# Performance work log

Measured on AMD Instinct MI355X. Metric: run time of the kernel, lower is better.

## Reference

```python
import jax, jax.numpy as jnp
import numpy as np

TWO_PI = 6.283185307179586


def setup_inputs() -> dict:
    key = jax.random.key(0)
    k1, k2, k3, k4, k5, k6 = jax.random.split(key, 6)
    B, T, D = 2, 8192, 1024
    x = jax.random.normal(k1, (B, T, D), dtype=jnp.float32)
    # nn.Linear weights are [out, in]; init with small scale like torch default
    s = 1.0 / np.sqrt(D)
    Wk = jax.random.uniform(k2, (D, D), jnp.float32, -s, s)
    Wv = jax.random.uniform(k3, (D, D), jnp.float32, -s, s)
    Wo = jax.random.uniform(k4, (D, D), jnp.float32, -s, s)
    # random phasor frequencies in [0, 2*pi)
    freqs = jax.random.uniform(k5, (D,), jnp.float32, 0.0, TWO_PI)
    return {"x": x, "Wk": Wk, "Wv": Wv, "Wo": Wo, "freqs": freqs}


def reference(x, Wk, Wv, Wo, freqs):
    B, T, C = x.shape
    # k projection is computed in the original forward but never used downstream
    k_real = x @ Wk.T  # [B,T,D] (dead value, kept for fidelity)
    v_real = x @ Wv.T  # [B,T,D]
    v = v_real.astype(jnp.complex64)
    # rotors: per-position unit phasors exp(i * t * freqs), shape [T, D]
    t = jnp.arange(T, dtype=jnp.float32)
    rotors = jnp.exp(1j * (t[:, None] * freqs[None, :])).astype(jnp.complex64)
    # bind each value with its rotor and accumulate causally (O(N) memory trace)
    memory_trace = jnp.cumsum(v * rotors[None, :, :], axis=1)  # [B,T,D] complex64
    # retrieve by unbinding with the conjugate rotor; take the real component
    retrieved = jnp.real(memory_trace * jnp.conj(rotors)[None, :, :])  # [B,T,D]
    return retrieved @ Wo.T
```

## Files before the change

### kernel.cpp

```cpp
#include <hip/hip_runtime.h>
#include <hip/hip_bf16.h>


#define B_  2
#define T_  8192
#define D_  1024
#define BT_ 16384
#define CS_ 64
#define NCHUNK_ 128

typedef __attribute__((ext_vector_type(4))) float f32x4;
typedef __attribute__((ext_vector_type(8))) short bf16x8;

static __device__ inline unsigned short f2bf(float f) {
    union { float f; unsigned int u; } a;
    a.f = f;
    unsigned int u = a.u;
    return (unsigned short)((u + 0x7FFFu + ((u >> 16) & 1u)) >> 16);
}
static __device__ inline float bf2f(unsigned short h) {
    union { unsigned int u; float f; } a;
    a.u = ((unsigned int)h) << 16;
    return a.f;
}

__global__ __launch_bounds__(256) void cast_all(const float* __restrict__ x,
                                                const float* __restrict__ Wv,
                                                const float* __restrict__ Wo,
                                                unsigned short* __restrict__ xb,
                                                unsigned short* __restrict__ wvb,
                                                unsigned short* __restrict__ wob) {
    const int nx = BT_ * D_ / 4;
    const int nw = D_ * D_ / 4;
    int i = blockIdx.x * 256 + threadIdx.x;
    const float4* src;
    unsigned short* dst;
    int j;
    if (i < nx)            { src = (const float4*)x;  dst = xb;  j = i; }
    else if (i < nx + nw)  { src = (const float4*)Wv; dst = wvb; j = i - nx; }
    else                   { src = (const float4*)Wo; dst = wob; j = i - nx - nw; }
    float4 v = src[j];
    ushort4 o;
    o.x = f2bf(v.x); o.y = f2bf(v.y); o.z = f2bf(v.z); o.w = f2bf(v.w);
    ((ushort4*)dst)[j] = o;
}

template <bool BF16OUT, bool FUSE_SUMS>
__global__ __launch_bounds__(256) void gemm_bt(const short* __restrict__ A,
                                               const short* __restrict__ Bm,
                                               void* __restrict__ Cout,
                                               const float* __restrict__ freqs,
                                               float* __restrict__ csum,
                                               int M, int N, int K) {
    __shared__ short lds[16384];
    const int lane = threadIdx.x & 63;
    const int wave = threadIdx.x >> 6;
    const int wr = wave >> 1, wc = wave & 1;

    const int nb = N >> 7;
    const int id = blockIdx.x;
    const int xcd = id & 7;
    const int slot = id >> 3;
    const int bn = (slot % nb) * 128;
    const int bm = (xcd * ((M >> 7) >> 3) + slot / nb) * 128;

    const int sr = lane >> 3;
    const int cb = lane & 7;
    const short* ga[4];
    const short* gb[4];
#pragma unroll
    for (int cc = 0; cc < 4; ++cc) {
        const int chunk = wave * 4 + cc;
        const int row = chunk * 8 + sr;
        const int col = (cb ^ (row & 7)) * 8;
        ga[cc] = A + (size_t)(bm + row) * K + col;
        gb[cc] = Bm + (size_t)(bn + row) * K + col;
    }

    const int c4r = lane >> 4;
    int aoff[4][2], boff[4][2];
#pragma unroll
    for (int i = 0; i < 4; ++i) {
        const int m = wr * 64 + (lane & 15) + i * 16;
        const int n = wc * 64 + (lane & 15) + i * 16;
#pragma unroll
        for (int ks = 0; ks < 2; ++ks) {
            aoff[i][ks] = m * 64 + (((ks * 4 + c4r) ^ (m & 7)) * 8);
            boff[i][ks] = 8192 + n * 64 + (((ks * 4 + c4r) ^ (n & 7)) * 8);
        }
    }

    f32x4 acc[4][4] = {};

    for (int k0 = 0; k0 < K; k0 += 64) {
#pragma unroll
        for (int cc = 0; cc < 4; ++cc) {
            const int chunk = wave * 4 + cc;
            __builtin_amdgcn_global_load_lds(
                (const __attribute__((address_space(1))) void*)(ga[cc] + k0),
                (__attribute__((address_space(3))) void*)&lds[chunk * 512], 16, 0, 0);
            __builtin_amdgcn_global_load_lds(
                (const __attribute__((address_space(1))) void*)(gb[cc] + k0),
                (__attribute__((address_space(3))) void*)&lds[8192 + chunk * 512], 16, 0, 0);
        }
        __syncthreads();
#pragma unroll
        for (int ks = 0; ks < 2; ++ks) {
            bf16x8 a[4], b[4];
#pragma unroll
            for (int i = 0; i < 4; ++i) a[i] = *(const bf16x8*)&lds[aoff[i][ks]];
#pragma unroll
            for (int j = 0; j < 4; ++j) b[j] = *(const bf16x8*)&lds[boff[j][ks]];
#pragma unroll
            for (int i = 0; i < 4; ++i)
#pragma unroll
                for (int j = 0; j < 4; ++j)
                    acc[i][j] = __builtin_amdgcn_mfma_f32_16x16x32_bf16(a[i], b[j], acc[i][j], 0, 0, 0);
        }
        __syncthreads();
    }

    const int row0 = c4r * 4;
#pragma unroll
    for (int i = 0; i < 4; ++i) {
#pragma unroll
        for (int j = 0; j < 4; ++j) {
            const int col = bn + wc * 64 + j * 16 + (lane & 15);
#pragma unroll
            for (int r = 0; r < 4; ++r) {
                const size_t row = bm + wr * 64 + i * 16 + row0 + r;
                if constexpr (BF16OUT)
                    ((unsigned short*)Cout)[row * N + col] = f2bf(acc[i][j][r]);
                else
                    ((float*)Cout)[row * N + col] = acc[i][j][r];
            }
        }
    }

    if constexpr (FUSE_SUMS) {
        const int b = bm >> 13;
        const int trow = bm & 8191;
        const int chunk = (trow >> 6) + wr;
        const int t0 = trow + wr * 64 + c4r * 4;
#pragma unroll
        for (int j = 0; j < 4; ++j) {
            const int d = bn + wc * 64 + j * 16 + (lane & 15);
            const float f = freqs[d];
            float ss, cc2;
            sincosf((float)t0 * f, &ss, &cc2);
            float s1, c1;
            sincosf(f, &s1, &c1);
            float c2 = c1 * c1 - s1 * s1, s2 = 2.f * c1 * s1;
            float c4 = c2 * c2 - s2 * s2, s4 = 2.f * c2 * s2;
            float c8 = c4 * c4 - s4 * s4, s8 = 2.f * c4 * s4;
            float c12 = c8 * c4 - s8 * s4, s12 = s8 * c4 + c8 * s4;
            float c13 = c12 * c1 - s12 * s1, s13 = s12 * c1 + c12 * s1;
            float ar = 0.f, ai = 0.f;
            float cr = cc2, sr2 = ss;
#pragma unroll
            for (int i = 0; i < 4; ++i) {
#pragma unroll
                for (int r = 0; r < 4; ++r) {
                    const float w = acc[i][j][r];
                    ar = fmaf(w, cr, ar); ai = fmaf(w, sr2, ai);
                    const float ec = (r < 3) ? c1 : c13;
                    const float es = (r < 3) ? s1 : s13;
                    const float nc = cr * ec - sr2 * es;
                    const float ns = sr2 * ec + cr * es;
                    cr = nc; sr2 = ns;
                }
            }
            ar += __shfl_xor(ar, 16); ai += __shfl_xor(ai, 16);
            ar += __shfl_xor(ar, 32); ai += __shfl_xor(ai, 32);
            if (c4r == 0)
                *(float2*)(csum + (((size_t)b * NCHUNK_ + chunk) * D_ + d) * 2) =
                    make_float2(ar, ai);
        }
    }
}

__global__ __launch_bounds__(256) void scan_pass2(float* __restrict__ csum) {
    const int g = blockIdx.x * 256 + threadIdx.x;
    const int b = g / D_;
    const int d = g % D_;
    float2* cs = (float2*)csum;
    const size_t base = (size_t)b * NCHUNK_ * D_ + d;
    float pr = 0.f, pi = 0.f;
    for (int cc = 0; cc < NCHUNK_; cc += 32) {
        float2 buf[32];
#pragma unroll
        for (int k = 0; k < 32; ++k) buf[k] = cs[base + (size_t)(cc + k) * D_];
#pragma unroll
        for (int k = 0; k < 32; ++k) {
            float r = buf[k].x, im = buf[k].y;
            buf[k] = make_float2(pr, pi);
            pr += r; pi += im;
        }
#pragma unroll
        for (int k = 0; k < 32; ++k) cs[base + (size_t)(cc + k) * D_] = buf[k];
    }
}

__global__ __launch_bounds__(256) void scan_pass3(const unsigned short* __restrict__ v,
                                                  const float* __restrict__ freqs,
                                                  const float* __restrict__ csum,
                                                  unsigned short* __restrict__ ret) {
    const int chunk = blockIdx.x;
    const int d0 = blockIdx.y * 512 + threadIdx.x * 2;
    const int b = blockIdx.z;

    float fr[2], s[2], c[2], sf[2], cf[2], ar[2], ai[2];
    {
        float2 f2 = *(const float2*)(freqs + d0);
        fr[0] = f2.x; fr[1] = f2.y;
    }
    const float t0f = (float)(chunk * CS_);
#pragma unroll
    for (int k = 0; k < 2; ++k) {
        sincosf(t0f * fr[k], &s[k], &c[k]);
        sincosf(fr[k], &sf[k], &cf[k]);
    }
    {
        const float4 o = *(const float4*)(csum + (((size_t)b * NCHUNK_ + chunk) * D_ + d0) * 2);
        ar[0] = o.x; ai[0] = o.y; ar[1] = o.z; ai[1] = o.w;
    }
    const unsigned int* vp = (const unsigned int*)(v + ((size_t)b * T_ + chunk * CS_) * D_ + d0);
    unsigned int* rp = (unsigned int*)(ret + ((size_t)b * T_ + chunk * CS_) * D_ + d0);
    for (int tb = 0; tb < CS_; tb += 8) {
        unsigned int w[8];
#pragma unroll
        for (int u = 0; u < 8; ++u) w[u] = vp[(size_t)(tb + u) * (D_ / 2)];
#pragma unroll
        for (int u = 0; u < 8; ++u) {
            float wv[2], o[2];
            wv[0] = bf2f((unsigned short)w[u]);
            wv[1] = bf2f((unsigned short)(w[u] >> 16));
#pragma unroll
            for (int k = 0; k < 2; ++k) {
                ar[k] = fmaf(wv[k], c[k], ar[k]);
                ai[k] = fmaf(wv[k], s[k], ai[k]);
                o[k] = ar[k] * c[k] + ai[k] * s[k];
                float nc = c[k] * cf[k] - s[k] * sf[k];
                float ns = s[k] * cf[k] + c[k] * sf[k];
                c[k] = nc; s[k] = ns;
            }
            rp[(size_t)(tb + u) * (D_ / 2)] =
                (unsigned int)f2bf(o[0]) | ((unsigned int)f2bf(o[1]) << 16);
        }
    }
}

extern "C" void kernel_launch(void* const* d_in, const int* in_sizes, int n_in,
                              void* d_out, int out_size, void* d_ws, size_t ws_size,
                              hipStream_t stream) {
    const float* x     = (const float*)d_in[0];
    const float* Wv    = (const float*)d_in[2];
    const float* Wo    = (const float*)d_in[3];
    const float* freqs = (const float*)d_in[4];
    float* out = (float*)d_out;

    char* ws = (char*)d_ws;
    unsigned short* x_bf  = (unsigned short*)ws;
    unsigned short* Wv_bf = (unsigned short*)(ws + 33554432);
    unsigned short* Wo_bf = (unsigned short*)(ws + 35651584);
    unsigned short* ret   = (unsigned short*)(ws + 37748736);
    float*          csum  = (float*)(ws + 71303168);
    unsigned short* v_bf = (unsigned short*)d_out;

    cast_all<<<(BT_ * D_ / 4 + 2 * D_ * D_ / 4) / 256, 256, 0, stream>>>(
        x, Wv, Wo, x_bf, Wv_bf, Wo_bf);

    gemm_bt<true, true><<<(BT_ / 128) * (D_ / 128), 256, 0, stream>>>(
        (const short*)x_bf, (const short*)Wv_bf, (void*)v_bf, freqs, csum, BT_, D_, D_);

    scan_pass2<<<(B_ * D_) / 256, 256, 0, stream>>>(csum);
    dim3 p3grid(NCHUNK_, D_ / 512, B_);
    scan_pass3<<<p3grid, 256, 0, stream>>>(v_bf, freqs, csum, ret);

    gemm_bt<false, false><<<(BT_ / 128) * (D_ / 128), 256, 0, stream>>>(
        (const short*)ret, (const short*)Wo_bf, (void*)out, nullptr, nullptr, BT_, D_, D_);
}
```

Baseline: 238.3 us.

## Enlarge GEMM tiles to 256x256 with double-buffered LDS prefetch pipeline

The bf16 GEMM kernel moves from 128x128 tiles with 4 waves to 256x256 tiles with 8 waves, each wave computing 128x64. LDS becomes a two-slot double buffer, and K-tiles are prefetched two steps ahead with explicit vmcnt waits, barriers and MFMA priority hints. This aims to raise data reuse per tile and hide global-load latency behind MFMA work. In exchange it uses 128KB LDS and many more accumulator registers, which lowers occupancy, and the grid shrinks to 256 blocks, which may not fill all CUs evenly.

```diff
diff --git a/kernel.cpp b/kernel.cpp
--- a/kernel.cpp
+++ b/kernel.cpp
@@ -46,89 +46,121 @@
 }
 
 template <bool BF16OUT, bool FUSE_SUMS>
-__global__ __launch_bounds__(256) void gemm_bt(const short* __restrict__ A,
-                                               const short* __restrict__ Bm,
-                                               void* __restrict__ Cout,
-                                               const float* __restrict__ freqs,
-                                               float* __restrict__ csum,
-                                               int M, int N, int K) {
-    __shared__ short lds[16384];
-    const int lane = threadIdx.x & 63;
-    const int wave = threadIdx.x >> 6;
-    const int wr = wave >> 1, wc = wave & 1;
-
-    const int nb = N >> 7;
+__global__ __launch_bounds__(512, 2) void gemm_bt(const short* __restrict__ A,
+                                                  const short* __restrict__ Bm,
+                                                  void* __restrict__ Cout,
+                                                  const float* __restrict__ freqs,
+                                                  float* __restrict__ csum,
+                                                  int M, int N, int K) {
+    __shared__ short lds[65536];
+    const int tid = threadIdx.x;
+    const int lane = tid & 63;
+    const int wave = tid >> 6;
+    const int wm = wave >> 2, wn = wave & 3;
+
+    const int nb = N >> 8;
     const int id = blockIdx.x;
     const int xcd = id & 7;
     const int slot = id >> 3;
-    const int bn = (slot % nb) * 128;
-    const int bm = (xcd * ((M >> 7) >> 3) + slot / nb) * 128;
-
-    const int sr = lane >> 3;
-    const int cb = lane & 7;
-    const short* ga[4];
-    const short* gb[4];
-#pragma unroll
-    for (int cc = 0; cc < 4; ++cc) {
-        const int chunk = wave * 4 + cc;
-        const int row = chunk * 8 + sr;
-        const int col = (cb ^ (row & 7)) * 8;
-        ga[cc] = A + (size_t)(bm + row) * K + col;
-        gb[cc] = Bm + (size_t)(bn + row) * K + col;
-    }
+    const int bn = (slot % nb) * 256;
+    const int bm = (xcd * ((M >> 8) >> 3) + slot / nb) * 256;
+
+    const int srow = lane >> 3;
+    const int sg = lane & 7;
+    const short* gsrc[8];
+#pragma unroll
+    for (int c = 0; c < 4; ++c) {
+        const int r = c * 64 + wave * 8 + srow;
+        const int col = (sg ^ (r & 7)) * 8;
+        gsrc[c]     = A  + (size_t)(bm + r) * K + col;
+        gsrc[c + 4] = Bm + (size_t)(bn + r) * K + col;
+    }
+
+    auto stage = [&](int kt, int sl) {
+        const int koff = kt * 64;
+        short* dstA = &lds[sl * 32768 + wave * 512];
+        short* dstB = &lds[sl * 32768 + 16384 + wave * 512];
+#pragma unroll
+        for (int c = 0; c < 4; ++c) {
+            __builtin_amdgcn_global_load_lds(
+                (const __attribute__((address_space(1))) void*)(gsrc[c] + koff),
+                (__attribute__((address_space(3))) void*)(dstA + c * 4096), 16, 0, 0);
+            __builtin_amdgcn_global_load_lds(
+                (const __attribute__((address_space(1))) void*)(gsrc[c + 4] + koff),
+                (__attribute__((address_space(3))) void*)(dstB + c * 4096), 16, 0, 0);
+        }
+    };
 
     const int c4r = lane >> 4;
-    int aoff[4][2], boff[4][2];
-#pragma unroll
-    for (int i = 0; i < 4; ++i) {
-        const int m = wr * 64 + (lane & 15) + i * 16;
-        const int n = wc * 64 + (lane & 15) + i * 16;
+    int aoff[8][2], boff[4][2];
+#pragma unroll
+    for (int i = 0; i < 8; ++i) {
+        const int m = wm * 128 + i * 16 + (lane & 15);
+#pragma unroll
+        for (int ks = 0; ks < 2; ++ks)
+            aoff[i][ks] = m * 64 + (((ks * 4 + c4r) ^ (m & 7)) * 8);
+    }
+#pragma unroll
+    for (int j = 0; j < 4; ++j) {
+        const int n = wn * 64 + j * 16 + (lane & 15);
+#pragma unroll
+        for (int ks = 0; ks < 2; ++ks)
+            boff[j][ks] = 16384 + n * 64 + (((ks * 4 + c4r) ^ (n & 7)) * 8);
+    }
+
+    f32x4 acc[8][4] = {};
+
+    stage(0, 0);
+    stage(1, 1);
+
+    const int NT = K >> 6;
+#pragma unroll 1
+    for (int t = 0; t < NT; ++t) {
+        if (t < NT - 1) asm volatile("s_waitcnt vmcnt(8)" ::: "memory");
+        else            asm volatile("s_waitcnt vmcnt(0)" ::: "memory");
+        __builtin_amdgcn_sched_barrier(0);
+        __builtin_amdgcn_s_barrier();
+        __builtin_amdgcn_sched_barrier(0);
+
+        const int sb = (t & 1) * 32768;
 #pragma unroll
         for (int ks = 0; ks < 2; ++ks) {
-            aoff[i][ks] = m * 64 + (((ks * 4 + c4r) ^ (m & 7)) * 8);
-            boff[i][ks] = 8192 + n * 64 + (((ks * 4 + c4r) ^ (n & 7)) * 8);
-        }
-    }
-
-    f32x4 acc[4][4] = {};
-
-    for (int k0 = 0; k0 < K; k0 += 64) {
-#pragma unroll
-        for (int cc = 0; cc < 4; ++cc) {
-            const int chunk = wave * 4 + cc;
-            __builtin_amdgcn_global_load_lds(
-                (const __attribute__((address_space(1))) void*)(ga[cc] + k0),
-                (__attribute__((address_space(3))) void*)&lds[chunk * 512], 16, 0, 0);
-            __builtin_amdgcn_global_load_lds(
-                (const __attribute__((address_space(1))) void*)(gb[cc] + k0),
-                (__attribute__((address_space(3))) void*)&lds[8192 + chunk * 512], 16, 0, 0);
-        }
-        __syncthreads();
-#pragma unroll
-        for (int ks = 0; ks < 2; ++ks) {
-            bf16x8 a[4], b[4];
-#pragma unroll
-            for (int i = 0; i < 4; ++i) a[i] = *(const bf16x8*)&lds[aoff[i][ks]];
-#pragma unroll
-            for (int j = 0; j < 4; ++j) b[j] = *(const bf16x8*)&lds[boff[j][ks]];
-#pragma unroll
-            for (int i = 0; i < 4; ++i)
-#pragma unroll
-                for (int j = 0; j < 4; ++j)
-                    acc[i][j] = __builtin_amdgcn_mfma_f32_16x16x32_bf16(a[i], b[j], acc[i][j], 0, 0, 0);
-        }
-        __syncthreads();
+            bf16x8 bb[4];
+#pragma unroll
+            for (int j = 0; j < 4; ++j)
+                bb[j] = *(const bf16x8*)&lds[sb + boff[j][ks]];
+#pragma unroll
+            for (int ih = 0; ih < 2; ++ih) {
+                bf16x8 aa[4];
+#pragma unroll
+                for (int ii = 0; ii < 4; ++ii)
+                    aa[ii] = *(const bf16x8*)&lds[sb + aoff[ih * 4 + ii][ks]];
+                __builtin_amdgcn_s_setprio(1);
+#pragma unroll
+                for (int ii = 0; ii < 4; ++ii)
+#pragma unroll
+                    for (int j = 0; j < 4; ++j)
+                        acc[ih * 4 + ii][j] = __builtin_amdgcn_mfma_f32_16x16x32_bf16(
+                            aa[ii], bb[j], acc[ih * 4 + ii][j], 0, 0, 0);
+                __builtin_amdgcn_s_setprio(0);
+            }
+        }
+        asm volatile("s_waitcnt lgkmcnt(0)" ::: "memory");
+        __builtin_amdgcn_sched_barrier(0);
+        __builtin_amdgcn_s_barrier();
+        __builtin_amdgcn_sched_barrier(0);
+        if (t < NT - 2) stage(t + 2, t & 1);
     }
 
     const int row0 = c4r * 4;
 #pragma unroll
-    for (int i = 0; i < 4; ++i) {
+    for (int i = 0; i < 8; ++i) {
 #pragma unroll
         for (int j = 0; j < 4; ++j) {
-            const int col = bn + wc * 64 + j * 16 + (lane & 15);
+            const int col = bn + wn * 64 + j * 16 + (lane & 15);
 #pragma unroll
             for (int r = 0; r < 4; ++r) {
-                const size_t row = bm + wr * 64 + i * 16 + row0 + r;
+                const size_t row = (size_t)bm + wm * 128 + i * 16 + row0 + r;
                 if constexpr (BF16OUT)
                     ((unsigned short*)Cout)[row * N + col] = f2bf(acc[i][j][r]);
                 else
@@ -140,41 +172,45 @@
     if constexpr (FUSE_SUMS) {
         const int b = bm >> 13;
         const int trow = bm & 8191;
-        const int chunk = (trow >> 6) + wr;
-        const int t0 = trow + wr * 64 + c4r * 4;
-#pragma unroll
-        for (int j = 0; j < 4; ++j) {
-            const int d = bn + wc * 64 + j * 16 + (lane & 15);
-            const float f = freqs[d];
-            float ss, cc2;
-            sincosf((float)t0 * f, &ss, &cc2);
-            float s1, c1;
-            sincosf(f, &s1, &c1);
-            float c2 = c1 * c1 - s1 * s1, s2 = 2.f * c1 * s1;
-            float c4 = c2 * c2 - s2 * s2, s4 = 2.f * c2 * s2;
-            float c8 = c4 * c4 - s4 * s4, s8 = 2.f * c4 * s4;
-            float c12 = c8 * c4 - s8 * s4, s12 = s8 * c4 + c8 * s4;
-            float c13 = c12 * c1 - s12 * s1, s13 = s12 * c1 + c12 * s1;
-            float ar = 0.f, ai = 0.f;
-            float cr = cc2, sr2 = ss;
-#pragma unroll
-            for (int i = 0; i < 4; ++i) {
-#pragma unroll
-                for (int r = 0; r < 4; ++r) {
-                    const float w = acc[i][j][r];
-                    ar = fmaf(w, cr, ar); ai = fmaf(w, sr2, ai);
-                    const float ec = (r < 3) ? c1 : c13;
-                    const float es = (r < 3) ? s1 : s13;
-                    const float nc = cr * ec - sr2 * es;
-                    const float ns = sr2 * ec + cr * es;
-                    cr = nc; sr2 = ns;
+#pragma unroll
+        for (int ig = 0; ig < 2; ++ig) {
+            const int chunk = (trow >> 6) + wm * 2 + ig;
+            const int t0 = trow + wm * 128 + ig * 64 + c4r * 4;
+#pragma unroll
+            for (int j = 0; j < 4; ++j) {
+                const int d = bn + wn * 64 + j * 16 + (lane & 15);
+                const float f = freqs[d];
+                float ss, cc2;
+                sincosf((float)t0 * f, &ss, &cc2);
+                float s1, c1;
+                sincosf(f, &s1, &c1);
+                float c2 = c1 * c1 - s1 * s1, s2 = 2.f * c1 * s1;
+                float c4 = c2 * c2 - s2 * s2, s4 = 2.f * c2 * s2;
+                float c8 = c4 * c4 - s4 * s4, s8 = 2.f * c4 * s4;
+                float c12 = c8 * c4 - s8 * s4, s12 = s8 * c4 + c8 * s4;
+                float c13 = c12 * c1 - s12 * s1, s13 = s12 * c1 + c12 * s1;
+                float ar = 0.f, ai = 0.f;
+                float cr = cc2, sr2 = ss;
+#pragma unroll
+                for (int ii = 0; ii < 4; ++ii) {
+                    const int i = ig * 4 + ii;
+#pragma unroll
+                    for (int r = 0; r < 4; ++r) {
+                        const float w = acc[i][j][r];
+                        ar = fmaf(w, cr, ar); ai = fmaf(w, sr2, ai);
+                        const float ec = (r < 3) ? c1 : c13;
+                        const float es = (r < 3) ? s1 : s13;
+                        const float nc = cr * ec - sr2 * es;
+                        const float ns = sr2 * ec + cr * es;
+                        cr = nc; sr2 = ns;
+                    }
                 }
+                ar += __shfl_xor(ar, 16); ai += __shfl_xor(ai, 16);
+                ar += __shfl_xor(ar, 32); ai += __shfl_xor(ai, 32);
+                if (c4r == 0)
+                    *(float2*)(csum + (((size_t)b * NCHUNK_ + chunk) * D_ + d) * 2) =
+                        make_float2(ar, ai);
             }
-            ar += __shfl_xor(ar, 16); ai += __shfl_xor(ai, 16);
-            ar += __shfl_xor(ar, 32); ai += __shfl_xor(ai, 32);
-            if (c4r == 0)
-                *(float2*)(csum + (((size_t)b * NCHUNK_ + chunk) * D_ + d) * 2) =
-                    make_float2(ar, ai);
         }
     }
 }
@@ -270,13 +306,13 @@
     cast_all<<<(BT_ * D_ / 4 + 2 * D_ * D_ / 4) / 256, 256, 0, stream>>>(
         x, Wv, Wo, x_bf, Wv_bf, Wo_bf);
 
-    gemm_bt<true, true><<<(BT_ / 128) * (D_ / 128), 256, 0, stream>>>(
+    gemm_bt<true, true><<<(BT_ / 256) * (D_ / 256), 512, 0, stream>>>(
         (const short*)x_bf, (const short*)Wv_bf, (void*)v_bf, freqs, csum, BT_, D_, D_);
 
     scan_pass2<<<(B_ * D_) / 256, 256, 0, stream>>>(csum);
     dim3 p3grid(NCHUNK_, D_ / 512, B_);
     scan_pass3<<<p3grid, 256, 0, stream>>>(v_bf, freqs, csum, ret);
 
-    gemm_bt<false, false><<<(BT_ / 128) * (D_ / 128), 256, 0, stream>>>(
+    gemm_bt<false, false><<<(BT_ / 256) * (D_ / 256), 512, 0, stream>>>(
         (const short*)ret, (const short*)Wo_bf, (void*)out, nullptr, nullptr, BT_, D_, D_);
 }
```

Measured after the change: 234.2 us. About the same (-1.7%).
